# Kernel tuning notes

Measured on AMD Instinct MI355X. Metric: run time of the kernel, lower is better.

## Reference

```python
import jax, jax.numpy as jnp
import numpy as np

N = 50000      # nodes
E = 800000     # edges
F_IN = 128     # num_node_features
H = 128        # hidden_channels
C = 10         # num_classes
G = 512        # graphs in batch


def setup_inputs() -> dict:
    key = jax.random.key(0)
    ks = jax.random.split(key, 8)
    x = jax.random.normal(ks[0], (N, F_IN), dtype=jnp.float32)
    edge_index = jax.random.randint(ks[1], (2, E), 0, N, dtype=jnp.int64)
    batch = jnp.sort(jax.random.randint(ks[2], (N,), 0, G, dtype=jnp.int64))
    s = 1.0 / np.sqrt(F_IN)
    W1 = jax.random.normal(ks[3], (F_IN, H), dtype=jnp.float32) * s
    b1 = jnp.zeros((H,), dtype=jnp.float32)
    W2 = jax.random.normal(ks[4], (H, H), dtype=jnp.float32) * s
    b2 = jnp.zeros((H,), dtype=jnp.float32)
    Wl = jax.random.normal(ks[5], (H, C), dtype=jnp.float32) * s
    bl = jnp.zeros((C,), dtype=jnp.float32)
    return {"x": x, "edge_index": edge_index, "batch": batch,
            "W1": W1, "b1": b1, "W2": W2, "b2": b2, "Wl": Wl, "bl": bl}


def _gcn_conv(h, src, dst, deg_inv_sqrt, W, b):
    # PyG GCNConv: x @ W, then symmetric-normalized scatter-add with self-loops.
    h = h @ W                                   # [N, H]
    norm = deg_inv_sqrt[src] * deg_inv_sqrt[dst]  # [E]
    msg = h[src] * norm[:, None]                # gather + scale, [E, H]
    out = jax.ops.segment_sum(msg, dst, num_segments=N)
    # self-loop contribution (deg already includes +1):
    out = out + h * (deg_inv_sqrt * deg_inv_sqrt)[:, None]
    return out + b


def reference(x, edge_index, batch, W1, b1, W2, b2, Wl, bl):
    src, dst = edge_index[0], edge_index[1]
    # degree on destination nodes, +1 for self-loops (PyG default)
    deg = jax.ops.segment_sum(jnp.ones((E,), x.dtype), dst, num_segments=N) + 1.0
    deg_inv_sqrt = jax.lax.rsqrt(deg)

    h = jax.nn.relu(_gcn_conv(x, src, dst, deg_inv_sqrt, W1, b1))
    h = jax.nn.relu(_gcn_conv(h, src, dst, deg_inv_sqrt, W2, b2))

    # global mean pool over graphs
    sums = jax.ops.segment_sum(h, batch, num_segments=G)          # [G, H]
    counts = jax.ops.segment_sum(jnp.ones((N,), h.dtype), batch, num_segments=G)
    pooled = sums / jnp.clip(counts, 1.0)[:, None]
    # dropout p=0.5 is identity in eval mode
    return pooled @ Wl + bl
```

## Files before the change

### kernel.cpp

```cpp
#include <hip/hip_runtime.h>
#include <hip/hip_bf16.h>
#include <hip/hip_fp16.h>

typedef unsigned short ushort_t;
typedef unsigned int uint32;
typedef __attribute__((ext_vector_type(8))) short short8;
typedef __attribute__((ext_vector_type(4))) float floatx4;

#define KMAX 64
#define BSHIFT 6
#define BCAP2 1280
#define MAXBUK 800

__device__ __forceinline__ float bf2f(ushort_t u) {
    return __uint_as_float(((uint32)u) << 16);
}
__device__ __forceinline__ ushort_t f2bf(float f) {
    uint32 x = __float_as_uint(f);
    return (ushort_t)((x + 0x7fffu + ((x >> 16) & 1u)) >> 16);
}
__device__ __forceinline__ uint32 pack2h(float a, float b) {
    return (uint32)__half_as_ushort(__float2half(a)) |
           ((uint32)__half_as_ushort(__float2half(b)) << 16);
}
__device__ __forceinline__ float2 unpack2h(uint32 q) {
    __half2 hh = *reinterpret_cast<__half2*>(&q);
    return __half22float2(hh);
}
__device__ __forceinline__ float h16f(ushort_t u) {
    __half h = *reinterpret_cast<__half*>(&u);
    return __half2float(h);
}

__global__ __launch_bounds__(256) void bin_k(const int* __restrict__ ei,
                                             int* __restrict__ bcur,
                                             uint32* __restrict__ binned,
                                             int E, int nbuk) {
    __shared__ int hist[MAXBUK], lbase[MAXBUK];
    int tid = threadIdx.x;
    for (int i = tid; i < nbuk; i += 256) hist[i] = 0;
    __syncthreads();
    int base = blockIdx.x * 4096;
    uint32 ed[16];
    int bk[16];
    #pragma unroll
    for (int i = 0; i < 16; ++i) {
        int e = base + i * 256 + tid;
        if (e < E) {
            int s = ei[e], d = ei[E + e];
            ed[i] = (uint32)s | ((uint32)d << 16);
            bk[i] = d >> BSHIFT;
            atomicAdd(&hist[bk[i]], 1);
        } else bk[i] = -1;
    }
    __syncthreads();
    for (int i = tid; i < nbuk; i += 256) lbase[i] = atomicAdd(&bcur[i], hist[i]);
    __syncthreads();
    for (int i = tid; i < nbuk; i += 256) hist[i] = 0;
    __syncthreads();
    #pragma unroll
    for (int i = 0; i < 16; ++i) {
        if (bk[i] >= 0) {
            int p = atomicAdd(&hist[bk[i]], 1);
            int idx = lbase[bk[i]] + p;
            if (idx < BCAP2) binned[(size_t)bk[i] * BCAP2 + idx] = ed[i];
        }
    }
}

__global__ __launch_bounds__(256) void fill4_k(const uint32* __restrict__ binned,
                                               const int* __restrict__ bcur,
                                               int* __restrict__ cnt,
                                               ushort_t* __restrict__ slot, int N) {
    __shared__ ushort_t ls[64 * KMAX];
    __shared__ int lc[64];
    int b = blockIdx.x;
    int tid = threadIdx.x;
    if (tid < 64) lc[tid] = 0;
    __syncthreads();
    int ne = bcur[b];
    if (ne > BCAP2) ne = BCAP2;
    const uint32* src = binned + (size_t)b * BCAP2;
    int nbase = b << BSHIFT;
    for (int i = tid; i < ne; i += 256) {
        uint32 ed = src[i];
        int s = (int)(ed & 0xFFFFu);
        int d = (int)(ed >> 16) - nbase;
        int p = atomicAdd(&lc[d], 1);
        if (p < KMAX) ls[(d << 6) + p] = (ushort_t)s;
    }
    __syncthreads();
    int nn = N - nbase;
    if (nn > 64) nn = 64;
    if (tid < 64 && tid < nn) cnt[nbase + tid] = lc[tid];
    uint4* gs = (uint4*)(slot + ((size_t)nbase << 6));
    const uint4* lsv = (const uint4*)ls;
    int totalv = nn * 8;
    for (int i = tid; i < totalv; i += 256) gs[i] = lsv[i];
}

__global__ __launch_bounds__(256) void gemm_k(const void* __restrict__ Av, int mode,
                                              const float* __restrict__ W,
                                              uint32* __restrict__ t2, int N,
                                              const int* __restrict__ cnt,
                                              const int* __restrict__ batch,
                                              int* __restrict__ gstart, int G,
                                              int do_bounds) {
    int tid = threadIdx.x;
    if (do_bounds) {
        int i = blockIdx.x * 256 + tid;
        if (i <= G) {
            int lo = 0, hi = N;
            while (lo < hi) {
                int mid = (lo + hi) >> 1;
                if (batch[mid] < i) lo = mid + 1; else hi = mid;
            }
            gstart[i] = lo;
        }
    }

    __shared__ ushort_t Wh[128][136];
    __shared__ ushort_t Wl[128][136];
    for (int i = tid; i < 128 * 128; i += 256) {
        int k = i >> 7, c = i & 127;
        float w = W[i];
        ushort_t h = f2bf(w);
        Wh[c][k] = h;
        Wl[c][k] = f2bf(w - bf2f(h));
    }
    __syncthreads();

    int wave = tid >> 6, lane = tid & 63;
    int row0 = blockIdx.x * 64 + wave * 16;
    int m = lane & 15;
    int arow = row0 + m;
    int koff = (lane >> 4) * 8;
    bool valid = arow < N;

    floatx4 acc[8];
    #pragma unroll
    for (int nt = 0; nt < 8; ++nt) acc[nt] = (floatx4){0.f, 0.f, 0.f, 0.f};

    for (int kk = 0; kk < 4; ++kk) {
        int k = kk * 32 + koff;
        short8 ah = (short8){0, 0, 0, 0, 0, 0, 0, 0};
        short8 al = (short8){0, 0, 0, 0, 0, 0, 0, 0};
        if (valid) {
            float v[8];
            if (mode == 0) {
                const float* p = (const float*)Av + (size_t)arow * 128 + k;
                floatx4 f0 = *(const floatx4*)p;
                floatx4 f1 = *(const floatx4*)(p + 4);
                v[0] = f0[0]; v[1] = f0[1]; v[2] = f0[2]; v[3] = f0[3];
                v[4] = f1[0]; v[5] = f1[1]; v[6] = f1[2]; v[7] = f1[3];
            } else {
                const uint32* hp = (const uint32*)Av + (size_t)arow * 64 + (k & 63);
                uint4 w0 = *(const uint4*)hp;
                uint4 w1 = *(const uint4*)(hp + 4);
                uint32 ws[8] = {w0.x, w0.y, w0.z, w0.w, w1.x, w1.y, w1.z, w1.w};
                bool hi = k >= 64;
                #pragma unroll
                for (int j = 0; j < 8; ++j) {
                    ushort_t u = hi ? (ushort_t)(ws[j] >> 16) : (ushort_t)(ws[j] & 0xFFFFu);
                    v[j] = fmaxf(h16f(u), 0.f);
                }
            }
            #pragma unroll
            for (int j = 0; j < 8; ++j) {
                ushort_t h = f2bf(v[j]);
                ah[j] = (short)h;
                al[j] = (short)f2bf(v[j] - bf2f(h));
            }
        }
        #pragma unroll
        for (int nt = 0; nt < 8; ++nt) {
            int col = nt * 16 + m;
            short8 bh = *(const short8*)(&Wh[col][k]);
            short8 bl = *(const short8*)(&Wl[col][k]);
            acc[nt] = __builtin_amdgcn_mfma_f32_16x16x32_bf16(ah, bh, acc[nt], 0, 0, 0);
            acc[nt] = __builtin_amdgcn_mfma_f32_16x16x32_bf16(al, bh, acc[nt], 0, 0, 0);
            acc[nt] = __builtin_amdgcn_mfma_f32_16x16x32_bf16(ah, bl, acc[nt], 0, 0, 0);
        }
    }

    int r0 = (lane >> 4) * 4;
    float dsc[4];
    #pragma unroll
    for (int r = 0; r < 4; ++r) {
        int row = row0 + r0 + r;
        dsc[r] = (row < N) ? rsqrtf((float)cnt[row] + 1.0f) : 0.f;
    }
    #pragma unroll
    for (int nt = 0; nt < 4; ++nt) {
        int c = nt * 16 + m;
        #pragma unroll
        for (int r = 0; r < 4; ++r) {
            int row = row0 + r0 + r;
            if (row < N)
                t2[(size_t)row * 64 + c] =
                    pack2h(acc[nt][r] * dsc[r], acc[nt + 4][r] * dsc[r]);
        }
    }
}

__global__ __launch_bounds__(256) void agg_k(const uint32* __restrict__ t2,
                                             const int* __restrict__ cnt,
                                             const ushort_t* __restrict__ slot,
                                             const float* __restrict__ bias,
                                             uint32* __restrict__ outp, int N) {
    int wave = threadIdx.x >> 6, lane = threadIdx.x & 63;
    int n = blockIdx.x * 4 + wave;
    if (n >= N) return;
    int deg = cnt[n];
    float d = rsqrtf((float)deg + 1.0f);
    if (deg > KMAX) deg = KMAX;
    float2 self = unpack2h(t2[(size_t)n * 64 + lane]);
    float acc0 = self.x;
    float acc1 = self.y;
    const ushort_t* sl = slot + (size_t)n * KMAX;
    int i = 0;
    for (; i + 16 <= deg; i += 16) {
        uint4 qa = *(const uint4*)(sl + i);
        uint4 qb = *(const uint4*)(sl + i + 8);
        uint32 sw[8] = {qa.x, qa.y, qa.z, qa.w, qb.x, qb.y, qb.z, qb.w};
        int s[16];
        #pragma unroll
        for (int u = 0; u < 8; ++u) {
            s[2 * u] = (int)(sw[u] & 0xFFFFu);
            s[2 * u + 1] = (int)(sw[u] >> 16);
        }
        float2 f[16];
        #pragma unroll
        for (int u = 0; u < 16; ++u)
            f[u] = unpack2h(t2[(size_t)s[u] * 64 + lane]);
        #pragma unroll
        for (int u = 0; u < 16; ++u) {
            acc0 += f[u].x;
            acc1 += f[u].y;
        }
    }
    for (; i + 4 <= deg; i += 4) {
        uint2 qa = *(const uint2*)(sl + i);
        int s[4] = {(int)(qa.x & 0xFFFFu), (int)(qa.x >> 16),
                    (int)(qa.y & 0xFFFFu), (int)(qa.y >> 16)};
        float2 f[4];
        #pragma unroll
        for (int u = 0; u < 4; ++u)
            f[u] = unpack2h(t2[(size_t)s[u] * 64 + lane]);
        #pragma unroll
        for (int u = 0; u < 4; ++u) {
            acc0 += f[u].x;
            acc1 += f[u].y;
        }
    }
    for (; i < deg; ++i) {
        float2 f = unpack2h(t2[(size_t)sl[i] * 64 + lane]);
        acc0 += f.x;
        acc1 += f.y;
    }
    acc0 = acc0 * d + bias[lane];
    acc1 = acc1 * d + bias[lane + 64];
    outp[(size_t)n * 64 + lane] = pack2h(acc0, acc1);
}

__global__ __launch_bounds__(256) void pool2_k(const uint32* __restrict__ h2,
                                               const int* __restrict__ gstart,
                                               const float* __restrict__ Wl,
                                               const float* __restrict__ bl,
                                               float* __restrict__ out, int C) {
    __shared__ float s0[256];
    __shared__ float s1[256];
    __shared__ float m[128];
    int g = blockIdx.x;
    int s = gstart[g], e = gstart[g + 1];
    int w = threadIdx.x & 63;
    int sub = threadIdx.x >> 6;
    float a0 = 0.f, a1 = 0.f;
    for (int n = s + sub; n < e; n += 4) {
        float2 f = unpack2h(h2[(size_t)n * 64 + w]);
        a0 += fmaxf(f.x, 0.f);
        a1 += fmaxf(f.y, 0.f);
    }
    s0[threadIdx.x] = a0;
    s1[threadIdx.x] = a1;
    __syncthreads();
    if (threadIdx.x < 64) {
        float inv = 1.f / fmaxf((float)(e - s), 1.f);
        m[w]      = (s0[w] + s0[w + 64] + s0[w + 128] + s0[w + 192]) * inv;
        m[w + 64] = (s1[w] + s1[w + 64] + s1[w + 128] + s1[w + 192]) * inv;
    }
    __syncthreads();
    if (threadIdx.x < C) {
        float sum = bl[threadIdx.x];
        #pragma unroll 4
        for (int jj = 0; jj < 128; ++jj)
            sum += m[jj] * Wl[jj * C + threadIdx.x];
        out[g * C + threadIdx.x] = sum;
    }
}

extern "C" void kernel_launch(void* const* d_in, const int* in_sizes, int n_in,
                              void* d_out, int out_size, void* d_ws, size_t ws_size,
                              hipStream_t stream) {
    const float* x   = (const float*)d_in[0];
    const int* ei    = (const int*)d_in[1];
    const int* batch = (const int*)d_in[2];
    const float* W1  = (const float*)d_in[3];
    const float* b1  = (const float*)d_in[4];
    const float* W2  = (const float*)d_in[5];
    const float* b2  = (const float*)d_in[6];
    const float* Wl  = (const float*)d_in[7];
    const float* bl  = (const float*)d_in[8];
    float* out = (float*)d_out;

    int N = in_sizes[2];
    int E = in_sizes[1] / 2;
    int C = in_sizes[8];
    int G = out_size / C;
    int nbuk = (N + 63) >> BSHIFT;

    char* w = (char*)d_ws;
    auto alloc = [&](size_t bytes) -> void* {
        void* p = (void*)w;
        w += (bytes + 255) & ~(size_t)255;
        return p;
    };
    int* bcur       = (int*)alloc((size_t)nbuk * 4);
    int* cnt        = (int*)alloc((size_t)N * 4);
    int* gstart     = (int*)alloc((size_t)(G + 1) * 4);
    ushort_t* slot  = (ushort_t*)alloc((size_t)nbuk * 64 * KMAX * 2);
    uint32* binned  = (uint32*)alloc((size_t)nbuk * BCAP2 * 4);
    uint32* t2      = (uint32*)alloc((size_t)N * 64 * 4);
    uint32* h1      = (uint32*)alloc((size_t)N * 64 * 4);
    uint32* h2      = (uint32*)alloc((size_t)N * 64 * 4);

    hipMemsetAsync(bcur, 0, (size_t)nbuk * 4, stream);

    int GB = (N + 63) / 64;
    int AB = (N + 3) / 4;
    int BB = (E + 4095) / 4096;

    bin_k<<<BB, 256, 0, stream>>>(ei, bcur, binned, E, nbuk);
    fill4_k<<<nbuk, 256, 0, stream>>>(binned, bcur, cnt, slot, N);
    gemm_k<<<GB, 256, 0, stream>>>((const void*)x, 0, W1, t2, N,
                                   cnt, batch, gstart, G, 1);
    agg_k<<<AB, 256, 0, stream>>>(t2, cnt, slot, b1, h1, N);
    gemm_k<<<GB, 256, 0, stream>>>((const void*)h1, 2, W2, t2, N,
                                   cnt, batch, gstart, G, 0);
    agg_k<<<AB, 256, 0, stream>>>(t2, cnt, slot, b2, h2, N);
    pool2_k<<<G, 256, 0, stream>>>(h2, gstart, Wl, bl, out, C);
}
```

Baseline: 234.2 us.

## Fuse graph build and first GEMM into persistent kernel with grid barriers

Merges the memset, edge binning, slot fill, graph-bounds search and first GEMM into one persistent kernel of 416 blocks, separated by a software grid barrier built on global atomics. The second aggregation and the mean pool are fused the same way, and the weight prep now uses vector loads. The aim is to remove kernel launch gaps and the tail idle time between small dependent kernels. In exchange, correctness depends on every block being co-resident, and the barriers add atomic spin cost while the persistent loops may lose occupancy.

```diff
diff --git a/kernel.cpp b/kernel.cpp
--- a/kernel.cpp
+++ b/kernel.cpp
@@ -11,6 +11,27 @@
 #define BSHIFT 6
 #define BCAP2 1280
 #define MAXBUK 800
+#define K1B 416
+#define K4B 1024
+
+__device__ unsigned g_cnt = 0;
+__device__ unsigned g_gen = 0;
+
+__device__ __forceinline__ void gbar(unsigned nb) {
+    __syncthreads();
+    if (threadIdx.x == 0) {
+        unsigned my = __hip_atomic_load(&g_gen, __ATOMIC_SEQ_CST, __HIP_MEMORY_SCOPE_AGENT);
+        unsigned old = __hip_atomic_fetch_add(&g_cnt, 1, __ATOMIC_SEQ_CST, __HIP_MEMORY_SCOPE_AGENT);
+        if (old == nb - 1) {
+            __hip_atomic_store(&g_cnt, 0u, __ATOMIC_SEQ_CST, __HIP_MEMORY_SCOPE_AGENT);
+            __hip_atomic_fetch_add(&g_gen, 1, __ATOMIC_SEQ_CST, __HIP_MEMORY_SCOPE_AGENT);
+        } else {
+            while (__hip_atomic_load(&g_gen, __ATOMIC_SEQ_CST, __HIP_MEMORY_SCOPE_AGENT) == my)
+                __builtin_amdgcn_s_sleep(2);
+        }
+    }
+    __syncthreads();
+}
 
 __device__ __forceinline__ float bf2f(ushort_t u) {
     return __uint_as_float(((uint32)u) << 16);
@@ -32,106 +53,29 @@
     return __half2float(h);
 }
 
-__global__ __launch_bounds__(256) void bin_k(const int* __restrict__ ei,
-                                             int* __restrict__ bcur,
-                                             uint32* __restrict__ binned,
-                                             int E, int nbuk) {
-    __shared__ int hist[MAXBUK], lbase[MAXBUK];
-    int tid = threadIdx.x;
-    for (int i = tid; i < nbuk; i += 256) hist[i] = 0;
-    __syncthreads();
-    int base = blockIdx.x * 4096;
-    uint32 ed[16];
-    int bk[16];
-    #pragma unroll
-    for (int i = 0; i < 16; ++i) {
-        int e = base + i * 256 + tid;
-        if (e < E) {
-            int s = ei[e], d = ei[E + e];
-            ed[i] = (uint32)s | ((uint32)d << 16);
-            bk[i] = d >> BSHIFT;
-            atomicAdd(&hist[bk[i]], 1);
-        } else bk[i] = -1;
-    }
-    __syncthreads();
-    for (int i = tid; i < nbuk; i += 256) lbase[i] = atomicAdd(&bcur[i], hist[i]);
-    __syncthreads();
-    for (int i = tid; i < nbuk; i += 256) hist[i] = 0;
-    __syncthreads();
-    #pragma unroll
-    for (int i = 0; i < 16; ++i) {
-        if (bk[i] >= 0) {
-            int p = atomicAdd(&hist[bk[i]], 1);
-            int idx = lbase[bk[i]] + p;
-            if (idx < BCAP2) binned[(size_t)bk[i] * BCAP2 + idx] = ed[i];
-        }
-    }
-}
-
-__global__ __launch_bounds__(256) void fill4_k(const uint32* __restrict__ binned,
-                                               const int* __restrict__ bcur,
-                                               int* __restrict__ cnt,
-                                               ushort_t* __restrict__ slot, int N) {
-    __shared__ ushort_t ls[64 * KMAX];
-    __shared__ int lc[64];
-    int b = blockIdx.x;
-    int tid = threadIdx.x;
-    if (tid < 64) lc[tid] = 0;
-    __syncthreads();
-    int ne = bcur[b];
-    if (ne > BCAP2) ne = BCAP2;
-    const uint32* src = binned + (size_t)b * BCAP2;
-    int nbase = b << BSHIFT;
-    for (int i = tid; i < ne; i += 256) {
-        uint32 ed = src[i];
-        int s = (int)(ed & 0xFFFFu);
-        int d = (int)(ed >> 16) - nbase;
-        int p = atomicAdd(&lc[d], 1);
-        if (p < KMAX) ls[(d << 6) + p] = (ushort_t)s;
-    }
-    __syncthreads();
-    int nn = N - nbase;
-    if (nn > 64) nn = 64;
-    if (tid < 64 && tid < nn) cnt[nbase + tid] = lc[tid];
-    uint4* gs = (uint4*)(slot + ((size_t)nbase << 6));
-    const uint4* lsv = (const uint4*)ls;
-    int totalv = nn * 8;
-    for (int i = tid; i < totalv; i += 256) gs[i] = lsv[i];
-}
-
-__global__ __launch_bounds__(256) void gemm_k(const void* __restrict__ Av, int mode,
-                                              const float* __restrict__ W,
-                                              uint32* __restrict__ t2, int N,
-                                              const int* __restrict__ cnt,
-                                              const int* __restrict__ batch,
-                                              int* __restrict__ gstart, int G,
-                                              int do_bounds) {
-    int tid = threadIdx.x;
-    if (do_bounds) {
-        int i = blockIdx.x * 256 + tid;
-        if (i <= G) {
-            int lo = 0, hi = N;
-            while (lo < hi) {
-                int mid = (lo + hi) >> 1;
-                if (batch[mid] < i) lo = mid + 1; else hi = mid;
-            }
-            gstart[i] = lo;
-        }
-    }
-
-    __shared__ ushort_t Wh[128][136];
-    __shared__ ushort_t Wl[128][136];
-    for (int i = tid; i < 128 * 128; i += 256) {
-        int k = i >> 7, c = i & 127;
-        float w = W[i];
-        ushort_t h = f2bf(w);
-        Wh[c][k] = h;
-        Wl[c][k] = f2bf(w - bf2f(h));
-    }
-    __syncthreads();
-
-    int wave = tid >> 6, lane = tid & 63;
-    int row0 = blockIdx.x * 64 + wave * 16;
+__device__ __forceinline__ void prep_w(const float* __restrict__ W,
+                                       ushort_t (*Wh)[136], ushort_t (*Wl)[136],
+                                       int tid) {
+    for (int i = tid; i < 128 * 32; i += 256) {
+        int k = i >> 5, c4 = (i & 31) << 2;
+        floatx4 w = *(const floatx4*)(W + k * 128 + c4);
+        #pragma unroll
+        for (int j = 0; j < 4; ++j) {
+            float ww = w[j];
+            ushort_t h = f2bf(ww);
+            Wh[c4 + j][k] = h;
+            Wl[c4 + j][k] = f2bf(ww - bf2f(h));
+        }
+    }
+}
+
+template <int MODE>
+__device__ __forceinline__ void gemm_tile(const void* __restrict__ Av,
+                                          const ushort_t (*Wh)[136],
+                                          const ushort_t (*Wl)[136],
+                                          const int* __restrict__ cnt,
+                                          uint32* __restrict__ t2, int N,
+                                          int row0, int lane) {
     int m = lane & 15;
     int arow = row0 + m;
     int koff = (lane >> 4) * 8;
@@ -147,7 +91,7 @@
         short8 al = (short8){0, 0, 0, 0, 0, 0, 0, 0};
         if (valid) {
             float v[8];
-            if (mode == 0) {
+            if (MODE == 0) {
                 const float* p = (const float*)Av + (size_t)arow * 128 + k;
                 floatx4 f0 = *(const floatx4*)p;
                 floatx4 f1 = *(const floatx4*)(p + 4);
@@ -203,14 +147,11 @@
     }
 }
 
-__global__ __launch_bounds__(256) void agg_k(const uint32* __restrict__ t2,
-                                             const int* __restrict__ cnt,
-                                             const ushort_t* __restrict__ slot,
-                                             const float* __restrict__ bias,
-                                             uint32* __restrict__ outp, int N) {
-    int wave = threadIdx.x >> 6, lane = threadIdx.x & 63;
-    int n = blockIdx.x * 4 + wave;
-    if (n >= N) return;
+__device__ __forceinline__ void agg_node(const uint32* __restrict__ t2,
+                                         const int* __restrict__ cnt,
+                                         const ushort_t* __restrict__ slot,
+                                         const float* __restrict__ bias,
+                                         uint32* __restrict__ outp, int n, int lane) {
     int deg = cnt[n];
     float d = rsqrtf((float)deg + 1.0f);
     if (deg > KMAX) deg = KMAX;
@@ -263,15 +204,149 @@
     outp[(size_t)n * 64 + lane] = pack2h(acc0, acc1);
 }
 
-__global__ __launch_bounds__(256) void pool2_k(const uint32* __restrict__ h2,
-                                               const int* __restrict__ gstart,
-                                               const float* __restrict__ Wl,
-                                               const float* __restrict__ bl,
-                                               float* __restrict__ out, int C) {
+__global__ __launch_bounds__(256, 2) void build_gemm1_k(
+    const int* __restrict__ ei, const int* __restrict__ batch,
+    const float* __restrict__ x, const float* __restrict__ W1,
+    int* __restrict__ bcur, int* __restrict__ cnt, int* __restrict__ gstart,
+    ushort_t* __restrict__ slot, uint32* __restrict__ binned,
+    uint32* __restrict__ t2, int N, int E, int G, int nbuk) {
+    __shared__ __align__(16) char smem[69632];
+    int tid = threadIdx.x;
+
+    for (int i = blockIdx.x * 256 + tid; i < nbuk; i += K1B * 256) bcur[i] = 0;
+    gbar(K1B);
+
+    {
+        int* hist = (int*)smem;
+        int* lbase = hist + MAXBUK;
+        int nch = (E + 4095) / 4096;
+        for (int ch = blockIdx.x; ch < nch; ch += K1B) {
+            for (int i = tid; i < nbuk; i += 256) hist[i] = 0;
+            __syncthreads();
+            int base = ch * 4096;
+            uint32 ed[16];
+            int bk[16];
+            #pragma unroll
+            for (int i = 0; i < 16; ++i) {
+                int e = base + i * 256 + tid;
+                if (e < E) {
+                    int s = ei[e], d = ei[E + e];
+                    ed[i] = (uint32)s | ((uint32)d << 16);
+                    bk[i] = d >> BSHIFT;
+                    atomicAdd(&hist[bk[i]], 1);
+                } else bk[i] = -1;
+            }
+            __syncthreads();
+            for (int i = tid; i < nbuk; i += 256) lbase[i] = atomicAdd(&bcur[i], hist[i]);
+            __syncthreads();
+            for (int i = tid; i < nbuk; i += 256) hist[i] = 0;
+            __syncthreads();
+            #pragma unroll
+            for (int i = 0; i < 16; ++i) {
+                if (bk[i] >= 0) {
+                    int p = atomicAdd(&hist[bk[i]], 1);
+                    int idx = lbase[bk[i]] + p;
+                    if (idx < BCAP2) binned[(size_t)bk[i] * BCAP2 + idx] = ed[i];
+                }
+            }
+            __syncthreads();
+        }
+    }
+    gbar(K1B);
+
+    {
+        ushort_t* ls = (ushort_t*)smem;
+        int* lc = (int*)(smem + 64 * KMAX * 2);
+        for (int b = blockIdx.x; b < nbuk; b += K1B) {
+            if (tid < 64) lc[tid] = 0;
+            __syncthreads();
+            int ne = bcur[b];
+            if (ne > BCAP2) ne = BCAP2;
+            const uint32* src = binned + (size_t)b * BCAP2;
+            int nbase = b << BSHIFT;
+            for (int i = tid; i < ne; i += 256) {
+                uint32 ed = src[i];
+                int s = (int)(ed & 0xFFFFu);
+                int d = (int)(ed >> 16) - nbase;
+                int p = atomicAdd(&lc[d], 1);
+                if (p < KMAX) ls[(d << 6) + p] = (ushort_t)s;
+            }
+            __syncthreads();
+            int nn = N - nbase;
+            if (nn > 64) nn = 64;
+            if (tid < 64 && tid < nn) cnt[nbase + tid] = lc[tid];
+            uint4* gs = (uint4*)(slot + ((size_t)nbase << 6));
+            const uint4* lsv = (const uint4*)ls;
+            int totalv = nn * 8;
+            for (int i = tid; i < totalv; i += 256) gs[i] = lsv[i];
+            __syncthreads();
+        }
+    }
+    gbar(K1B);
+
+    for (int i = blockIdx.x * 256 + tid; i <= G; i += K1B * 256) {
+        int lo = 0, hi = N;
+        while (lo < hi) {
+            int mid = (lo + hi) >> 1;
+            if (batch[mid] < i) lo = mid + 1; else hi = mid;
+        }
+        gstart[i] = lo;
+    }
+    {
+        ushort_t (*Wh)[136] = (ushort_t (*)[136])smem;
+        ushort_t (*Wl)[136] = (ushort_t (*)[136])(smem + 34816);
+        prep_w(W1, Wh, Wl, tid);
+        __syncthreads();
+        int wave = tid >> 6, lane = tid & 63;
+        int ntile = (N + 63) >> 6;
+        for (int t = blockIdx.x; t < ntile; t += K1B)
+            gemm_tile<0>((const void*)x, Wh, Wl, cnt, t2, N, t * 64 + wave * 16, lane);
+    }
+}
+
+__global__ __launch_bounds__(256) void agg_k(const uint32* __restrict__ t2,
+                                             const int* __restrict__ cnt,
+                                             const ushort_t* __restrict__ slot,
+                                             const float* __restrict__ bias,
+                                             uint32* __restrict__ outp, int N) {
+    int wave = threadIdx.x >> 6, lane = threadIdx.x & 63;
+    int n = blockIdx.x * 4 + wave;
+    if (n >= N) return;
+    agg_node(t2, cnt, slot, bias, outp, n, lane);
+}
+
+__global__ __launch_bounds__(256) void gemm2_k(const uint32* __restrict__ h1,
+                                               const float* __restrict__ W2,
+                                               const int* __restrict__ cnt,
+                                               uint32* __restrict__ t2, int N) {
+    __shared__ ushort_t Wh[128][136];
+    __shared__ ushort_t Wl[128][136];
+    int tid = threadIdx.x;
+    prep_w(W2, Wh, Wl, tid);
+    __syncthreads();
+    int wave = tid >> 6, lane = tid & 63;
+    gemm_tile<2>((const void*)h1, Wh, Wl, cnt, t2, N,
+                 blockIdx.x * 64 + wave * 16, lane);
+}
+
+__global__ __launch_bounds__(256, 4) void agg2_pool_k(
+    const uint32* __restrict__ t2, const int* __restrict__ cnt,
+    const ushort_t* __restrict__ slot, const float* __restrict__ bias,
+    uint32* __restrict__ h2, const int* __restrict__ gstart,
+    const float* __restrict__ Wl, const float* __restrict__ bl,
+    float* __restrict__ out, int N, int C, int G) {
     __shared__ float s0[256];
     __shared__ float s1[256];
     __shared__ float m[128];
+    int wave = threadIdx.x >> 6, lane = threadIdx.x & 63;
+    int AB = (N + 3) / 4;
+    for (int c = blockIdx.x; c < AB; c += K4B) {
+        int n = c * 4 + wave;
+        if (n < N) agg_node(t2, cnt, slot, bias, h2, n, lane);
+    }
+    gbar(K4B);
     int g = blockIdx.x;
+    if (g >= G) return;
     int s = gstart[g], e = gstart[g + 1];
     int w = threadIdx.x & 63;
     int sub = threadIdx.x >> 6;
@@ -334,19 +409,13 @@
     uint32* h1      = (uint32*)alloc((size_t)N * 64 * 4);
     uint32* h2      = (uint32*)alloc((size_t)N * 64 * 4);
 
-    hipMemsetAsync(bcur, 0, (size_t)nbuk * 4, stream);
-
     int GB = (N + 63) / 64;
     int AB = (N + 3) / 4;
-    int BB = (E + 4095) / 4096;
-
-    bin_k<<<BB, 256, 0, stream>>>(ei, bcur, binned, E, nbuk);
-    fill4_k<<<nbuk, 256, 0, stream>>>(binned, bcur, cnt, slot, N);
-    gemm_k<<<GB, 256, 0, stream>>>((const void*)x, 0, W1, t2, N,
-                                   cnt, batch, gstart, G, 1);
+
+    build_gemm1_k<<<K1B, 256, 0, stream>>>(ei, batch, x, W1, bcur, cnt, gstart,
+                                           slot, binned, t2, N, E, G, nbuk);
     agg_k<<<AB, 256, 0, stream>>>(t2, cnt, slot, b1, h1, N);
-    gemm_k<<<GB, 256, 0, stream>>>((const void*)h1, 2, W2, t2, N,
-                                   cnt, batch, gstart, G, 0);
-    agg_k<<<AB, 256, 0, stream>>>(t2, cnt, slot, b2, h2, N);
-    pool2_k<<<G, 256, 0, stream>>>(h2, gstart, Wl, bl, out, C);
-}
+    gemm2_k<<<GB, 256, 0, stream>>>(h1, W2, cnt, t2, N);
+    agg2_pool_k<<<K4B, 256, 0, stream>>>(t2, cnt, slot, b2, h2, gstart,
+                                         Wl, bl, out, N, C, G);
+}
```

Result: slower. 703.1 us (+200.2%).

## Fuse memset, binning and slot fill into one persistent kernel with grid barriers

Applied to the files above, without the earlier changes.

Replaces the memset plus the bin_k and fill4_k launches with a single build_k kernel. It zeroes the bucket counters, bins the edges, then fills the per-node slots, and separates the phases with a software grid-wide barrier built on global atomics. This removes two launch gaps and the memset. In exchange, the barrier assumes all nbuk (782) blocks are co-resident, which launch_bounds(256,4) makes plausible on this GPU, and the global barrier counters persist across launches. The W staging in gemm_k also now loads W as float4 vectors.

```diff
diff --git a/kernel.cpp b/kernel.cpp
--- a/kernel.cpp
+++ b/kernel.cpp
@@ -12,6 +12,25 @@
 #define BCAP2 1280
 #define MAXBUK 800
 
+__device__ unsigned g_cnt = 0;
+__device__ unsigned g_gen = 0;
+
+__device__ __forceinline__ void gbar(unsigned nb) {
+    __syncthreads();
+    if (threadIdx.x == 0) {
+        unsigned my = __hip_atomic_load(&g_gen, __ATOMIC_SEQ_CST, __HIP_MEMORY_SCOPE_AGENT);
+        unsigned old = __hip_atomic_fetch_add(&g_cnt, 1, __ATOMIC_SEQ_CST, __HIP_MEMORY_SCOPE_AGENT);
+        if (old == nb - 1) {
+            __hip_atomic_store(&g_cnt, 0u, __ATOMIC_SEQ_CST, __HIP_MEMORY_SCOPE_AGENT);
+            __hip_atomic_fetch_add(&g_gen, 1, __ATOMIC_SEQ_CST, __HIP_MEMORY_SCOPE_AGENT);
+        } else {
+            while (__hip_atomic_load(&g_gen, __ATOMIC_SEQ_CST, __HIP_MEMORY_SCOPE_AGENT) == my)
+                __builtin_amdgcn_s_sleep(2);
+        }
+    }
+    __syncthreads();
+}
+
 __device__ __forceinline__ float bf2f(ushort_t u) {
     return __uint_as_float(((uint32)u) << 16);
 }
@@ -32,71 +51,83 @@
     return __half2float(h);
 }
 
-__global__ __launch_bounds__(256) void bin_k(const int* __restrict__ ei,
-                                             int* __restrict__ bcur,
-                                             uint32* __restrict__ binned,
-                                             int E, int nbuk) {
-    __shared__ int hist[MAXBUK], lbase[MAXBUK];
+__global__ __launch_bounds__(256, 4) void build_k(
+    const int* __restrict__ ei, int* __restrict__ bcur, int* __restrict__ cnt,
+    ushort_t* __restrict__ slot, uint32* __restrict__ binned,
+    int N, int E, int nbuk) {
+    __shared__ __align__(16) char smem[8704];
     int tid = threadIdx.x;
-    for (int i = tid; i < nbuk; i += 256) hist[i] = 0;
-    __syncthreads();
-    int base = blockIdx.x * 4096;
-    uint32 ed[16];
-    int bk[16];
-    #pragma unroll
-    for (int i = 0; i < 16; ++i) {
-        int e = base + i * 256 + tid;
-        if (e < E) {
-            int s = ei[e], d = ei[E + e];
-            ed[i] = (uint32)s | ((uint32)d << 16);
-            bk[i] = d >> BSHIFT;
-            atomicAdd(&hist[bk[i]], 1);
-        } else bk[i] = -1;
-    }
-    __syncthreads();
-    for (int i = tid; i < nbuk; i += 256) lbase[i] = atomicAdd(&bcur[i], hist[i]);
-    __syncthreads();
-    for (int i = tid; i < nbuk; i += 256) hist[i] = 0;
-    __syncthreads();
-    #pragma unroll
-    for (int i = 0; i < 16; ++i) {
-        if (bk[i] >= 0) {
-            int p = atomicAdd(&hist[bk[i]], 1);
-            int idx = lbase[bk[i]] + p;
-            if (idx < BCAP2) binned[(size_t)bk[i] * BCAP2 + idx] = ed[i];
-        }
-    }
-}
-
-__global__ __launch_bounds__(256) void fill4_k(const uint32* __restrict__ binned,
-                                               const int* __restrict__ bcur,
-                                               int* __restrict__ cnt,
-                                               ushort_t* __restrict__ slot, int N) {
-    __shared__ ushort_t ls[64 * KMAX];
-    __shared__ int lc[64];
-    int b = blockIdx.x;
-    int tid = threadIdx.x;
-    if (tid < 64) lc[tid] = 0;
-    __syncthreads();
-    int ne = bcur[b];
-    if (ne > BCAP2) ne = BCAP2;
-    const uint32* src = binned + (size_t)b * BCAP2;
-    int nbase = b << BSHIFT;
-    for (int i = tid; i < ne; i += 256) {
-        uint32 ed = src[i];
-        int s = (int)(ed & 0xFFFFu);
-        int d = (int)(ed >> 16) - nbase;
-        int p = atomicAdd(&lc[d], 1);
-        if (p < KMAX) ls[(d << 6) + p] = (ushort_t)s;
-    }
-    __syncthreads();
-    int nn = N - nbase;
-    if (nn > 64) nn = 64;
-    if (tid < 64 && tid < nn) cnt[nbase + tid] = lc[tid];
-    uint4* gs = (uint4*)(slot + ((size_t)nbase << 6));
-    const uint4* lsv = (const uint4*)ls;
-    int totalv = nn * 8;
-    for (int i = tid; i < totalv; i += 256) gs[i] = lsv[i];
+    unsigned nb = gridDim.x;
+
+    for (int i = blockIdx.x * 256 + tid; i < nbuk; i += nb * 256) bcur[i] = 0;
+    gbar(nb);
+
+    {
+        int* hist = (int*)smem;
+        int* lbase = (int*)(smem + 4352);
+        int nch = (E + 4095) / 4096;
+        for (int ch = blockIdx.x; ch < nch; ch += nb) {
+            for (int i = tid; i < nbuk; i += 256) hist[i] = 0;
+            __syncthreads();
+            int base = ch * 4096;
+            uint32 ed[16];
+            int bk[16];
+            #pragma unroll
+            for (int i = 0; i < 16; ++i) {
+                int e = base + i * 256 + tid;
+                if (e < E) {
+                    int s = ei[e], d = ei[E + e];
+                    ed[i] = (uint32)s | ((uint32)d << 16);
+                    bk[i] = d >> BSHIFT;
+                    atomicAdd(&hist[bk[i]], 1);
+                } else bk[i] = -1;
+            }
+            __syncthreads();
+            for (int i = tid; i < nbuk; i += 256) lbase[i] = atomicAdd(&bcur[i], hist[i]);
+            __syncthreads();
+            for (int i = tid; i < nbuk; i += 256) hist[i] = 0;
+            __syncthreads();
+            #pragma unroll
+            for (int i = 0; i < 16; ++i) {
+                if (bk[i] >= 0) {
+                    int p = atomicAdd(&hist[bk[i]], 1);
+                    int idx = lbase[bk[i]] + p;
+                    if (idx < BCAP2) binned[(size_t)bk[i] * BCAP2 + idx] = ed[i];
+                }
+            }
+            __syncthreads();
+        }
+    }
+    gbar(nb);
+
+    {
+        ushort_t* ls = (ushort_t*)smem;
+        int* lc = (int*)(smem + 64 * KMAX * 2);
+        for (int b = blockIdx.x; b < nbuk; b += nb) {
+            if (tid < 64) lc[tid] = 0;
+            __syncthreads();
+            int ne = bcur[b];
+            if (ne > BCAP2) ne = BCAP2;
+            const uint32* src = binned + (size_t)b * BCAP2;
+            int nbase = b << BSHIFT;
+            for (int i = tid; i < ne; i += 256) {
+                uint32 ed = src[i];
+                int s = (int)(ed & 0xFFFFu);
+                int d = (int)(ed >> 16) - nbase;
+                int p = atomicAdd(&lc[d], 1);
+                if (p < KMAX) ls[(d << 6) + p] = (ushort_t)s;
+            }
+            __syncthreads();
+            int nn = N - nbase;
+            if (nn > 64) nn = 64;
+            if (tid < 64 && tid < nn) cnt[nbase + tid] = lc[tid];
+            uint4* gs = (uint4*)(slot + ((size_t)nbase << 6));
+            const uint4* lsv = (const uint4*)ls;
+            int totalv = nn * 8;
+            for (int i = tid; i < totalv; i += 256) gs[i] = lsv[i];
+            __syncthreads();
+        }
+    }
 }
 
 __global__ __launch_bounds__(256) void gemm_k(const void* __restrict__ Av, int mode,
@@ -121,12 +152,16 @@
 
     __shared__ ushort_t Wh[128][136];
     __shared__ ushort_t Wl[128][136];
-    for (int i = tid; i < 128 * 128; i += 256) {
-        int k = i >> 7, c = i & 127;
-        float w = W[i];
-        ushort_t h = f2bf(w);
-        Wh[c][k] = h;
-        Wl[c][k] = f2bf(w - bf2f(h));
+    for (int i = tid; i < 128 * 32; i += 256) {
+        int k = i >> 5, c4 = (i & 31) << 2;
+        floatx4 w = *(const floatx4*)(W + k * 128 + c4);
+        #pragma unroll
+        for (int j = 0; j < 4; ++j) {
+            float ww = w[j];
+            ushort_t h = f2bf(ww);
+            Wh[c4 + j][k] = h;
+            Wl[c4 + j][k] = f2bf(ww - bf2f(h));
+        }
     }
     __syncthreads();
 
@@ -334,14 +369,10 @@
     uint32* h1      = (uint32*)alloc((size_t)N * 64 * 4);
     uint32* h2      = (uint32*)alloc((size_t)N * 64 * 4);
 
-    hipMemsetAsync(bcur, 0, (size_t)nbuk * 4, stream);
-
     int GB = (N + 63) / 64;
     int AB = (N + 3) / 4;
-    int BB = (E + 4095) / 4096;
-
-    bin_k<<<BB, 256, 0, stream>>>(ei, bcur, binned, E, nbuk);
-    fill4_k<<<nbuk, 256, 0, stream>>>(binned, bcur, cnt, slot, N);
+
+    build_k<<<nbuk, 256, 0, stream>>>(ei, bcur, cnt, slot, binned, N, E, nbuk);
     gemm_k<<<GB, 256, 0, stream>>>((const void*)x, 0, W1, t2, N,
                                    cnt, batch, gstart, G, 1);
     agg_k<<<AB, 256, 0, stream>>>(t2, cnt, slot, b1, h1, N);
```

New measurement: 494.3 us. 111% more time.
